# Optimization experiments

Hardware: AMD Instinct MI355X
Metric: run time of the kernel (lower is better)

The kernel has to match this reference:

```python
import jax, jax.numpy as jnp
import numpy as np


def _ln(x, g, b, eps=1e-5):
    m = x.mean(-1, keepdims=True)
    v = x.var(-1, keepdims=True)
    return (x - m) / jnp.sqrt(v + eps) * g + b


def _causal_linear_attn(q, k, v, eps=1e-3):
    # q, k, v: (b, h, n, d). Matches lucidrains causal_linear_attn with bucket_size=1:
    # q -> softmax over feature dim, k -> exp, inclusive cumsum of k and k(outer)v over n.
    dh = q.shape[-1]
    q = jax.nn.softmax(q, axis=-1) * (dh ** -0.5)
    k = jnp.exp(k)
    k_cum = jnp.cumsum(k, axis=2)                                  # (b,h,n,d)
    ctx = jnp.cumsum(k[..., :, None] * v[..., None, :], axis=2)    # (b,h,n,d,d) running sum of k_i v_i^T
    d_inv = 1.0 / jnp.clip(jnp.einsum('bhnd,bhnd->bhn', k_cum, q), eps, None)
    return jnp.einsum('bhnd,bhnde->bhne', q, ctx) * d_inv[..., None]


def reference(x, ln1_g, ln1_b, Wq, Wk, Wv, Wo, bo, ln2_g, ln2_b, W1, b1, W2, b2, n_heads):
    depth = Wq.shape[0]
    B, N, D = x.shape
    H = int(n_heads)
    dh = D // H
    for i in range(depth):
        # --- pre-norm linear self-attention block ---
        xn = _ln(x, ln1_g[i], ln1_b[i])
        q = (xn @ Wq[i]).reshape(B, N, H, dh).transpose(0, 2, 1, 3)
        k = (xn @ Wk[i]).reshape(B, N, H, dh).transpose(0, 2, 1, 3)
        v = (xn @ Wv[i]).reshape(B, N, H, dh).transpose(0, 2, 1, 3)
        a = _causal_linear_attn(q, k, v)
        a = a.transpose(0, 2, 1, 3).reshape(B, N, D)
        x = x + a @ Wo[i] + bo[i]
        # --- pre-norm feed-forward block (mult=4, exact GELU) ---
        xn = _ln(x, ln2_g[i], ln2_b[i])
        x = x + jax.nn.gelu(xn @ W1[i] + b1[i], approximate=False) @ W2[i] + b2[i]
    return x


def setup_inputs() -> dict:
    key = jax.random.key(0)
    ks = jax.random.split(key, 8)
    B, N, D, H, depth = 2, 2048, 1024, 16, 2
    FF = 4 * D
    s = D ** -0.5
    x = jax.random.normal(ks[0], (B, N, D), dtype=jnp.float32)
    Wq = jax.random.normal(ks[1], (depth, D, D), dtype=jnp.float32) * s
    Wk = jax.random.normal(ks[2], (depth, D, D), dtype=jnp.float32) * s
    Wv = jax.random.normal(ks[3], (depth, D, D), dtype=jnp.float32) * s
    Wo = jax.random.normal(ks[4], (depth, D, D), dtype=jnp.float32) * s
    W1 = jax.random.normal(ks[5], (depth, D, FF), dtype=jnp.float32) * s
    W2 = jax.random.normal(ks[6], (depth, FF, D), dtype=jnp.float32) * (FF ** -0.5)
    return dict(
        x=x,
        ln1_g=jnp.ones((depth, D), jnp.float32), ln1_b=jnp.zeros((depth, D), jnp.float32),
        Wq=Wq, Wk=Wk, Wv=Wv, Wo=Wo, bo=jnp.zeros((depth, D), jnp.float32),
        ln2_g=jnp.ones((depth, D), jnp.float32), ln2_b=jnp.zeros((depth, D), jnp.float32),
        W1=W1, b1=jnp.zeros((depth, FF), jnp.float32),
        W2=W2, b2=jnp.zeros((depth, D), jnp.float32),
        n_heads=H,
    )
```

## Files before the change

kernel.cpp:

```cpp
#include <hip/hip_runtime.h>
#include <cmath>

#define BB 2
#define SEQ 2048
#define DIM 1024
#define NH 16
#define DH 64
#define DEPTH 2
#define FFD 4096
#define CHK 64
#define NCHK (SEQ/CHK)
#define ROWS (BB*SEQ)
#define QKP (3*DIM)

typedef __bf16 bf16x8 __attribute__((ext_vector_type(8)));
typedef __bf16 bf16x4 __attribute__((ext_vector_type(4)));
typedef float  f32x4  __attribute__((ext_vector_type(4)));

#define AS1 __attribute__((address_space(1)))
#define AS3 __attribute__((address_space(3)))
#define FENCE() asm volatile("" ::: "memory")
#define WAIT_LGKM0_NOPIN() asm volatile("s_waitcnt lgkmcnt(0)" ::: "memory")

__device__ __forceinline__ float gelu_fast(float x) {
    float x3 = x * x * x;
    float y = 1.5957691216057308f * (x + 0.044715f * x3);
    return x * __builtin_amdgcn_rcpf(1.0f + __expf(-y));
}

__device__ __forceinline__ int swz128(int row, int col) {
    return row * 64 + (col ^ ((row & 7) << 3));
}

__device__ __forceinline__ void swz_tile(int bid, int NX, int NY, int& tx, int& ty) {
    int NB = NX * NY;
    int q = NB >> 3, r = NB & 7;
    int xcd = bid & 7, seq = bid >> 3;
    int start = (xcd < r) ? xcd * (q + 1) : r * (q + 1) + (xcd - r) * q;
    int wgid = start + seq;
    int g = 0, rem = wgid;
    int gw = (NX < 4) ? NX : 4;
    while (rem >= gw * NY) {
        rem -= gw * NY; g++;
        int left = NX - 4 * g;
        gw = left < 4 ? left : 4;
    }
    ty = rem / gw;
    tx = 4 * g + rem % gw;
}

__global__ __launch_bounds__(256) void ln_kernel(
    const float* __restrict__ x, const float* __restrict__ g,
    const float* __restrict__ b, __bf16* __restrict__ out)
{
    int row = blockIdx.x;
    const float4* xr = (const float4*)(x + (size_t)row * DIM);
    int t = threadIdx.x;
    float4 v = xr[t];
    float s  = v.x + v.y + v.z + v.w;
    float ss = v.x*v.x + v.y*v.y + v.z*v.z + v.w*v.w;
    #pragma unroll
    for (int off = 32; off > 0; off >>= 1) {
        s  += __shfl_down(s, off);
        ss += __shfl_down(ss, off);
    }
    __shared__ float wsum[4], wsq[4], stats[2];
    int wid = t >> 6, lane = t & 63;
    if (lane == 0) { wsum[wid] = s; wsq[wid] = ss; }
    __syncthreads();
    if (t == 0) {
        float S  = wsum[0] + wsum[1] + wsum[2] + wsum[3];
        float SS = wsq[0] + wsq[1] + wsq[2] + wsq[3];
        float mean = S * (1.0f / DIM);
        float var  = SS * (1.0f / DIM) - mean * mean;
        stats[0] = mean;
        stats[1] = rsqrtf(var + 1e-5f);
    }
    __syncthreads();
    float mean = stats[0], rstd = stats[1];
    float4 gv = ((const float4*)g)[t];
    float4 bv = ((const float4*)b)[t];
    bf16x4 o;
    o[0] = (__bf16)((v.x - mean) * rstd * gv.x + bv.x);
    o[1] = (__bf16)((v.y - mean) * rstd * gv.y + bv.y);
    o[2] = (__bf16)((v.z - mean) * rstd * gv.z + bv.z);
    o[3] = (__bf16)((v.w - mean) * rstd * gv.w + bv.w);
    *(bf16x4*)(out + (size_t)row * DIM + t * 4) = o;
}

__global__ __launch_bounds__(256) void transpose_all(
    const float* __restrict__ wq, const float* __restrict__ wk,
    const float* __restrict__ wv, const float* __restrict__ wo,
    const float* __restrict__ w1, const float* __restrict__ w2,
    __bf16* __restrict__ wqkt, __bf16* __restrict__ wot,
    __bf16* __restrict__ w1t, __bf16* __restrict__ w2t)
{
    int id = blockIdx.x;
    const float* W; __bf16* Wt; int K, N, txt, tyt;
    if (id < 4096) {
        int seg = id >> 10, r = id & 1023;
        K = DIM; N = DIM;
        txt = r & 31; tyt = r >> 5;
        W  = seg == 0 ? wq : seg == 1 ? wk : seg == 2 ? wv : wo;
        Wt = seg < 3 ? wqkt + (size_t)seg * DIM * DIM : wot;
    } else if (id < 8192) {
        int r = id - 4096;
        K = DIM; N = FFD;
        txt = r & 127; tyt = r >> 7;
        W = w1; Wt = w1t;
    } else {
        int r = id - 8192;
        K = FFD; N = DIM;
        txt = r & 31; tyt = r >> 5;
        W = w2; Wt = w2t;
    }
    __shared__ float tile[32][33];
    int bx = txt * 32, by = tyt * 32;
    int tx = threadIdx.x & 31, ty = threadIdx.x >> 5;
    #pragma unroll
    for (int i = 0; i < 32; i += 8)
        tile[ty + i][tx] = W[(size_t)(by + ty + i) * N + bx + tx];
    __syncthreads();
    #pragma unroll
    for (int i = 0; i < 32; i += 8)
        Wt[(size_t)(bx + ty + i) * K + by + tx] = (__bf16)tile[tx][ty + i];
}

__global__ __launch_bounds__(256) void transpose_v(
    const __bf16* __restrict__ qkv, __bf16* __restrict__ vT)
{
    __shared__ __bf16 tile[64 * 64];
    int bx = blockIdx.x;
    int by = blockIdx.y;
    int t = threadIdx.x;
    int r0 = t >> 3, sl = t & 7;
    #pragma unroll
    for (int i = 0; i < 2; i++) {
        int row = i * 32 + r0;
        bf16x8 d = *(const bf16x8*)(qkv + (size_t)(bx * 64 + row) * QKP + 2 * DIM + by * 64 + sl * 8);
        *(bf16x8*)&tile[row * 64 + ((sl ^ (row & 7)) << 3)] = d;
    }
    __syncthreads();
    #pragma unroll
    for (int i = 0; i < 2; i++) {
        int d = i * 32 + r0;
        int rbase = sl * 8;
        bf16x8 o;
        #pragma unroll
        for (int j = 0; j < 8; j++) {
            int rr = rbase + j;
            o[j] = tile[rr * 64 + (((((d >> 3)) ^ (rr & 7)) << 3) | (d & 7))];
        }
        *(bf16x8*)(vT + (size_t)(by * 64 + d) * ROWS + bx * 64 + rbase) = o;
    }
}

#define TBM 256
#define TBN 256
#define TBK 64
template<int MODE, int OUTBF>
__global__ __launch_bounds__(512) void gemm256(
    const __bf16* __restrict__ A, const __bf16* __restrict__ Bt,
    void* __restrict__ Cv, const float* __restrict__ bias,
    const float* __restrict__ res, int M, int N, int K, int Kp,
    int NXT, int NYT, int NS)
{
    __shared__ __bf16 lds[2][2][TBM * TBK];
    int nb = NXT * NYT;
    int sk = blockIdx.x / nb;
    int tx, ty;
    swz_tile(blockIdx.x % nb, NXT, NYT, tx, ty);
    if (NS > 1) {
        A  += (size_t)sk * K;
        Bt += (size_t)sk * K;
        Cv = (void*)((char*)Cv + (size_t)sk * M * N * (OUTBF ? 2 : 4));
    }
    const int bm = ty * TBM, bn = tx * TBN;
    const int t = threadIdx.x;
    const int l = t & 63, w = t >> 6;
    const int wm = w >> 2, wn = w & 3;
    const int lm = l & 15, lk = l >> 4;

    f32x4 acc[8][4] = {};
    const int nt = K / TBK;
    const int NIT = nt / 2;

    const int s7 = lm & 7;
    const int c0 = (lk ^ s7) << 3;
    const int c1 = ((4 ^ lk) ^ s7) << 3;
    const __bf16* pA[2][2] = {
        { &lds[0][0][(wm * 128 + lm) * 64 + c0], &lds[0][0][(wm * 128 + lm) * 64 + c1] },
        { &lds[1][0][(wm * 128 + lm) * 64 + c0], &lds[1][0][(wm * 128 + lm) * 64 + c1] } };
    const __bf16* pB[2][2] = {
        { &lds[0][1][(wn * 64 + lm) * 64 + c0], &lds[0][1][(wn * 64 + lm) * 64 + c1] },
        { &lds[1][1][(wn * 64 + lm) * 64 + c0], &lds[1][1][(wn * 64 + lm) * 64 + c1] } };

    const int srow0 = t >> 3;
    const int scol0 = ((t & 7) ^ (srow0 & 7)) * 8;
    const __bf16* gAb = A + (size_t)(bm + srow0) * Kp + scol0;
    const __bf16* gBb = Bt + (size_t)(bn + srow0) * Kp + scol0;
    const int ldsw = w * 512;

    auto STAGEH = [&](int bf, int mat, int hf, int kt) {
        const __bf16* srcb = mat ? gBb : gAb;
        #pragma unroll
        for (int i = 0; i < 2; i++) {
            __builtin_amdgcn_global_load_lds(
                (const AS1 void*)(srcb + (size_t)(hf * 128 + i * 64) * Kp + kt * 64),
                (AS3 void*)(&lds[bf][mat][(hf * 2 + i) * 4096 + ldsw]), 16, 0, 0);
        }
    };
    auto LDA = [&](int bf, int g, bf16x8* af) {
        #pragma unroll
        for (int j = 0; j < 4; j++) {
            af[j * 2 + 0] = *(const bf16x8*)(pA[bf][0] + (g * 4 + j) * 1024);
            af[j * 2 + 1] = *(const bf16x8*)(pA[bf][1] + (g * 4 + j) * 1024);
        }
    };
    auto LDB = [&](int bf, bf16x8* bfv) {
        #pragma unroll
        for (int n = 0; n < 4; n++) {
            bfv[n * 2 + 0] = *(const bf16x8*)(pB[bf][0] + n * 1024);
            bfv[n * 2 + 1] = *(const bf16x8*)(pB[bf][1] + n * 1024);
        }
    };
    auto MM = [&](int g, int ng, bf16x8* af, bf16x8* bfv) {
        __builtin_amdgcn_s_setprio(1);
        #pragma unroll
        for (int j = 0; j < 4; j++)
            #pragma unroll
            for (int nn = 0; nn < 2; nn++)
                #pragma unroll
                for (int kk = 0; kk < 2; kk++)
                    acc[g * 4 + j][ng * 2 + nn] = __builtin_amdgcn_mfma_f32_16x16x32_bf16(
                        af[j * 2 + kk], bfv[(ng * 2 + nn) * 2 + kk], acc[g * 4 + j][ng * 2 + nn], 0, 0, 0);
        __builtin_amdgcn_s_setprio(0);
    };

    STAGEH(0, 0, 0, 0); STAGEH(0, 0, 1, 0); STAGEH(0, 1, 0, 0); STAGEH(0, 1, 1, 0);
    STAGEH(1, 1, 0, 1); STAGEH(1, 1, 1, 1); STAGEH(1, 0, 0, 1);
    asm volatile("s_waitcnt vmcnt(6)" ::: "memory");
    __builtin_amdgcn_s_barrier();

    bf16x8 aF[8], bF[8];
    for (int it = 0; it < NIT; it++) {
        int T2 = 2 * it + 2, U2 = 2 * it + 3;
        LDA(0, 0, aF); LDB(0, bF);
        STAGEH(1, 0, 1, 2 * it + 1);
        FENCE(); __builtin_amdgcn_s_barrier();
        MM(0, 0, aF, bF);
        WAIT_LGKM0_NOPIN();
        FENCE(); __builtin_amdgcn_s_barrier();
        if (T2 < nt) STAGEH(0, 1, 0, T2);
        FENCE(); __builtin_amdgcn_s_barrier();
        MM(0, 1, aF, bF);
        FENCE(); __builtin_amdgcn_s_barrier();
        LDA(0, 1, aF);
        if (T2 < nt) STAGEH(0, 1, 1, T2);
        FENCE(); __builtin_amdgcn_s_barrier();
        MM(1, 1, aF, bF);
        FENCE(); __builtin_amdgcn_s_barrier();
        if (T2 < nt) {
            STAGEH(0, 0, 0, T2);
            asm volatile("s_waitcnt vmcnt(6)" ::: "memory");
        } else {
            asm volatile("s_waitcnt vmcnt(0)" ::: "memory");
        }
        __builtin_amdgcn_s_barrier();
        MM(1, 0, aF, bF);
        FENCE(); __builtin_amdgcn_s_barrier();
        LDA(1, 0, aF); LDB(1, bF);
        if (T2 < nt) STAGEH(0, 0, 1, T2);
        FENCE(); __builtin_amdgcn_s_barrier();
        MM(0, 0, aF, bF);
        WAIT_LGKM0_NOPIN();
        FENCE(); __builtin_amdgcn_s_barrier();
        if (U2 < nt) STAGEH(1, 1, 0, U2);
        FENCE(); __builtin_amdgcn_s_barrier();
        MM(0, 1, aF, bF);
        FENCE(); __builtin_amdgcn_s_barrier();
        LDA(1, 1, aF);
        if (U2 < nt) STAGEH(1, 1, 1, U2);
        FENCE(); __builtin_amdgcn_s_barrier();
        MM(1, 1, aF, bF);
        FENCE(); __builtin_amdgcn_s_barrier();
        if (U2 < nt) {
            STAGEH(1, 0, 0, U2);
            asm volatile("s_waitcnt vmcnt(6)" ::: "memory");
        } else {
            asm volatile("s_waitcnt vmcnt(0)" ::: "memory");
        }
        __builtin_amdgcn_s_barrier();
        MM(1, 0, aF, bF);
        FENCE(); __builtin_amdgcn_s_barrier();
    }

    #pragma unroll
    for (int m = 0; m < 8; m++) {
        #pragma unroll
        for (int n = 0; n < 4; n++) {
            int col = bn + wn * 64 + n * 16 + lm;
            #pragma unroll
            for (int r = 0; r < 4; r++) {
                int row = bm + wm * 128 + m * 16 + lk * 4 + r;
                float v = acc[m][n][r];
                if (MODE == 1) v += res[(size_t)row * N + col] + bias[col];
                if (MODE == 2) v = gelu_fast(v + bias[col]);
                if (OUTBF) ((__bf16*)Cv)[(size_t)row * N + col] = (__bf16)v;
                else       ((float*)Cv)[(size_t)row * N + col] = v;
            }
        }
    }
}

template<int DOLN>
__global__ __launch_bounds__(256) void reduce4ln(
    const __bf16* __restrict__ parts, const float* __restrict__ bias,
    float* __restrict__ x, const float* __restrict__ g,
    const float* __restrict__ b, __bf16* __restrict__ xn)
{
    const size_t PS = (size_t)ROWS * DIM;
    int row = blockIdx.x, t = threadIdx.x;
    size_t base = (size_t)row * DIM + t * 4;
    float4 xr = *(const float4*)(x + base);
    float4 bv = ((const float4*)bias)[t];
    float o0 = xr.x + bv.x, o1 = xr.y + bv.y, o2 = xr.z + bv.z, o3 = xr.w + bv.w;
    #pragma unroll
    for (int s = 0; s < 4; s++) {
        bf16x4 p = *(const bf16x4*)(parts + s * PS + base);
        o0 += (float)p[0]; o1 += (float)p[1]; o2 += (float)p[2]; o3 += (float)p[3];
    }
    float4 o = {o0, o1, o2, o3};
    *(float4*)(x + base) = o;
    if constexpr (DOLN) {
        float s  = o0 + o1 + o2 + o3;
        float ss = o0*o0 + o1*o1 + o2*o2 + o3*o3;
        #pragma unroll
        for (int off = 32; off > 0; off >>= 1) {
            s  += __shfl_down(s, off);
            ss += __shfl_down(ss, off);
        }
        __shared__ float wsum[4], wsq[4], stats[2];
        int wid = t >> 6, lane = t & 63;
        if (lane == 0) { wsum[wid] = s; wsq[wid] = ss; }
        __syncthreads();
        if (t == 0) {
            float S  = wsum[0] + wsum[1] + wsum[2] + wsum[3];
            float SS = wsq[0] + wsq[1] + wsq[2] + wsq[3];
            float mean = S * (1.0f / DIM);
            float var  = SS * (1.0f / DIM) - mean * mean;
            stats[0] = mean;
            stats[1] = rsqrtf(var + 1e-5f);
        }
        __syncthreads();
        float mean = stats[0], rstd = stats[1];
        float4 gv = ((const float4*)g)[t];
        float4 bvv = ((const float4*)b)[t];
        bf16x4 on;
        on[0] = (__bf16)((o0 - mean) * rstd * gv.x + bvv.x);
        on[1] = (__bf16)((o1 - mean) * rstd * gv.y + bvv.y);
        on[2] = (__bf16)((o2 - mean) * rstd * gv.z + bvv.z);
        on[3] = (__bf16)((o3 - mean) * rstd * gv.w + bvv.w);
        *(bf16x4*)(xn + base) = on;
    }
}

__global__ __launch_bounds__(256) void attn_local_m(
    const __bf16* __restrict__ qkv, const __bf16* __restrict__ vTg,
    float* __restrict__ KVT, float* __restrict__ Ksum)
{
    int blk = blockIdx.x;
    int c = blk % NCHK, bh = blk / NCHK;
    int b = bh / NH, h = bh % NH;
    __shared__ __bf16 ek_s[64 * 64];
    __shared__ __bf16 ekT_s[64 * 68];
    __shared__ float ksum_p[4][64];
    int t = threadIdx.x, w = t >> 6, l = t & 63;
    size_t rowbase = (size_t)(b * SEQ + c * CHK);

    {
        int m = t >> 2, dq = t & 3;
        const __bf16* kr = qkv + (rowbase + m) * QKP + DIM + h * DH + dq * 16;
        bf16x8 k0 = *(const bf16x8*)kr;
        bf16x8 k1 = *(const bf16x8*)(kr + 8);
        bf16x8 e0, e1;
        #pragma unroll
        for (int j = 0; j < 8; j++) {
            e0[j] = (__bf16)__expf((float)k0[j]);
            e1[j] = (__bf16)__expf((float)k1[j]);
        }
        *(bf16x8*)&ek_s[swz128(m, dq * 16)] = e0;
        *(bf16x8*)&ek_s[swz128(m, dq * 16 + 8)] = e1;
    }
    __syncthreads();
    {
        float kacc = 0.f;
        #pragma unroll
        for (int g = 0; g < 4; g++) {
            bf16x4 pk;
            #pragma unroll
            for (int j = 0; j < 4; j++) {
                __bf16 e = ek_s[swz128(w * 16 + g * 4 + j, l)];
                pk[j] = e;
                kacc += (float)e;
            }
            *(bf16x4*)&ekT_s[l * 68 + w * 16 + g * 4] = pk;
        }
        ksum_p[w][l] = kacc;
    }
    __syncthreads();
    f32x4 acc[4] = {};
    const __bf16* vbase = vTg + (size_t)(h * DH + w * 16 + (l & 15)) * ROWS
                        + (size_t)b * SEQ + c * CHK + (l >> 4) * 8;
    bf16x8 a0 = *(const bf16x8*)vbase;
    bf16x8 a1 = *(const bf16x8*)(vbase + 32);
    #pragma unroll
    for (int fn = 0; fn < 4; fn++) {
        int rbase = (fn * 16 + (l & 15)) * 68 + (l >> 4) * 8;
        bf16x4 b0a = *(const bf16x4*)&ekT_s[rbase];
        bf16x4 b0b = *(const bf16x4*)&ekT_s[rbase + 4];
        bf16x4 b1a = *(const bf16x4*)&ekT_s[rbase + 32];
        bf16x4 b1b = *(const bf16x4*)&ekT_s[rbase + 36];
        bf16x8 b0, b1;
        #pragma unroll
        for (int j = 0; j < 4; j++) {
            b0[j] = b0a[j]; b0[j + 4] = b0b[j];
            b1[j] = b1a[j]; b1[j + 4] = b1b[j];
        }
        acc[fn] = __builtin_amdgcn_mfma_f32_16x16x32_bf16(a0, b0, acc[fn], 0, 0, 0);
        acc[fn] = __builtin_amdgcn_mfma_f32_16x16x32_bf16(a1, b1, acc[fn], 0, 0, 0);
    }
    float* kvout = KVT + (size_t)(bh * NCHK + c) * (DH * DH);
    #pragma unroll
    for (int fn = 0; fn < 4; fn++)
        #pragma unroll
        for (int r = 0; r < 4; r++)
            kvout[(w * 16 + (l >> 4) * 4 + r) * DH + fn * 16 + (l & 15)] = acc[fn][r];
    if (t < 64) {
        float s = ksum_p[0][t] + ksum_p[1][t] + ksum_p[2][t] + ksum_p[3][t];
        Ksum[(size_t)(bh * NCHK + c) * DH + t] = s;
    }
}

__global__ __launch_bounds__(256) void attn_scan2(
    float* __restrict__ KV, float* __restrict__ Ksum)
{
    int bh = blockIdx.y;
    int bx = blockIdx.x;
    int t = threadIdx.x;
    if (bx < 16) {
        int elem = bx * 256 + t;
        float run = 0.f;
        for (int c = 0; c < NCHK; c++) {
            float* p = KV + ((size_t)(bh * NCHK + c)) * (DH * DH) + elem;
            float tmp = *p;
            *p = run;
            run += tmp;
        }
    } else if (t < DH) {
        float run = 0.f;
        for (int c = 0; c < NCHK; c++) {
            float* p = Ksum + ((size_t)(bh * NCHK + c)) * DH + t;
            float tmp = *p;
            *p = run;
            run += tmp;
        }
    }
}

__global__ __launch_bounds__(256) void attn_out_m(
    const __bf16* __restrict__ qkv, const __bf16* __restrict__ vTg,
    const float* __restrict__ KVT, const float* __restrict__ Ksum,
    __bf16* __restrict__ ag)
{
    int blk = blockIdx.x;
    int c = blk % NCHK, bh = blk / NCHK;
    int b = bh / NH, h = bh % NH;
    __shared__ __bf16 q_s[64 * 64];
    __shared__ __bf16 ek_s[64 * 64];
    __shared__ __bf16 s_s[64 * 64];
    __shared__ __bf16 kvT_s[64 * 64];
    __shared__ float denom_s[64];
    int t = threadIdx.x, w = t >> 6, l = t & 63;
    size_t rowbase = (size_t)(b * SEQ + c * CHK);

    {
        int i = t >> 2, dq = t & 3;
        const __bf16* qr = qkv + (rowbase + i) * QKP + h * DH + dq * 16;
        bf16x8 q0 = *(const bf16x8*)qr, q1 = *(const bf16x8*)(qr + 8);
        float qf[16];
        #pragma unroll
        for (int j = 0; j < 8; j++) { qf[j] = (float)q0[j]; qf[8 + j] = (float)q1[j]; }
        float mx = qf[0];
        #pragma unroll
        for (int j = 1; j < 16; j++) mx = fmaxf(mx, qf[j]);
        mx = fmaxf(mx, __shfl_xor(mx, 1));
        mx = fmaxf(mx, __shfl_xor(mx, 2));
        float ss = 0.f;
        #pragma unroll
        for (int j = 0; j < 16; j++) { qf[j] = __expf(qf[j] - mx); ss += qf[j]; }
        ss += __shfl_xor(ss, 1);
        ss += __shfl_xor(ss, 2);
        float sc = 0.125f / ss;
        bf16x8 o0, o1;
        #pragma unroll
        for (int j = 0; j < 8; j++) {
            o0[j] = (__bf16)(qf[j] * sc);
            o1[j] = (__bf16)(qf[8 + j] * sc);
        }
        *(bf16x8*)&q_s[swz128(i, dq * 16)] = o0;
        *(bf16x8*)&q_s[swz128(i, dq * 16 + 8)] = o1;
        const float* kp = Ksum + (size_t)(bh * NCHK + c) * DH + dq * 16;
        float dk = 0.f;
        #pragma unroll
        for (int j = 0; j < 16; j++) dk += (qf[j] * sc) * kp[j];
        dk += __shfl_xor(dk, 1);
        dk += __shfl_xor(dk, 2);
        if (dq == 0) denom_s[i] = dk;
    }
    {
        int m = t >> 2, dq = t & 3;
        const __bf16* kr = qkv + (rowbase + m) * QKP + DIM + h * DH + dq * 16;
        bf16x8 k0 = *(const bf16x8*)kr, k1 = *(const bf16x8*)(kr + 8);
        bf16x8 e0, e1;
        #pragma unroll
        for (int j = 0; j < 8; j++) {
            e0[j] = (__bf16)__expf((float)k0[j]);
            e1[j] = (__bf16)__expf((float)k1[j]);
        }
        *(bf16x8*)&ek_s[swz128(m, dq * 16)] = e0;
        *(bf16x8*)&ek_s[swz128(m, dq * 16 + 8)] = e1;
    }
    {
        int e = t >> 2, dq = t & 3;
        const float* kvr = KVT + (size_t)(bh * NCHK + c) * (DH * DH) + e * DH + dq * 16;
        bf16x8 o0, o1;
        #pragma unroll
        for (int j = 0; j < 8; j++) { o0[j] = (__bf16)kvr[j]; o1[j] = (__bf16)kvr[8 + j]; }
        *(bf16x8*)&kvT_s[swz128(e, dq * 16)] = o0;
        *(bf16x8*)&kvT_s[swz128(e, dq * 16 + 8)] = o1;
    }
    __syncthreads();

    bf16x8 bq0 = *(const bf16x8*)&q_s[swz128(w * 16 + (l & 15), (l >> 4) * 8)];
    bf16x8 bq1 = *(const bf16x8*)&q_s[swz128(w * 16 + (l & 15), 32 + (l >> 4) * 8)];
    int i_col = w * 16 + (l & 15);
    float dsum = 0.f;
    #pragma unroll
    for (int fm = 0; fm < 4; fm++) {
        bf16x8 ae0 = *(const bf16x8*)&ek_s[swz128(fm * 16 + (l & 15), (l >> 4) * 8)];
        bf16x8 ae1 = *(const bf16x8*)&ek_s[swz128(fm * 16 + (l & 15), 32 + (l >> 4) * 8)];
        f32x4 z = {};
        z = __builtin_amdgcn_mfma_f32_16x16x32_bf16(ae0, bq0, z, 0, 0, 0);
        z = __builtin_amdgcn_mfma_f32_16x16x32_bf16(ae1, bq1, z, 0, 0, 0);
        bf16x4 pk;
        #pragma unroll
        for (int r = 0; r < 4; r++) {
            int m = fm * 16 + (l >> 4) * 4 + r;
            float v = (m <= i_col) ? z[r] : 0.f;
            pk[r] = (__bf16)v;
            dsum += (float)pk[r];
        }
        *(bf16x4*)&s_s[swz128(i_col, fm * 16 + (l >> 4) * 4)] = pk;
    }
    dsum += __shfl_xor(dsum, 16);
    dsum += __shfl_xor(dsum, 32);
    if (l < 16) denom_s[w * 16 + l] += dsum;

    bf16x8 as0 = *(const bf16x8*)&s_s[swz128(w * 16 + (l & 15), (l >> 4) * 8)];
    bf16x8 as1 = *(const bf16x8*)&s_s[swz128(w * 16 + (l & 15), 32 + (l >> 4) * 8)];
    f32x4 oacc[4] = {};
    #pragma unroll
    for (int fn = 0; fn < 4; fn++) {
        const __bf16* vb = vTg + (size_t)(h * DH + fn * 16 + (l & 15)) * ROWS
                         + (size_t)b * SEQ + c * CHK + (l >> 4) * 8;
        bf16x8 bv0 = *(const bf16x8*)vb;
        bf16x8 bv1 = *(const bf16x8*)(vb + 32);
        bf16x8 bk0 = *(const bf16x8*)&kvT_s[swz128(fn * 16 + (l & 15), (l >> 4) * 8)];
        bf16x8 bk1 = *(const bf16x8*)&kvT_s[swz128(fn * 16 + (l & 15), 32 + (l >> 4) * 8)];
        f32x4 z = oacc[fn];
        z = __builtin_amdgcn_mfma_f32_16x16x32_bf16(as0, bv0, z, 0, 0, 0);
        z = __builtin_amdgcn_mfma_f32_16x16x32_bf16(as1, bv1, z, 0, 0, 0);
        z = __builtin_amdgcn_mfma_f32_16x16x32_bf16(bq0, bk0, z, 0, 0, 0);
        z = __builtin_amdgcn_mfma_f32_16x16x32_bf16(bq1, bk1, z, 0, 0, 0);
        oacc[fn] = z;
    }
    #pragma unroll
    for (int r = 0; r < 4; r++) {
        int i = w * 16 + (l >> 4) * 4 + r;
        float dinv = 1.0f / fmaxf(denom_s[i], 1e-3f);
        #pragma unroll
        for (int fn = 0; fn < 4; fn++)
            ag[(rowbase + i) * DIM + h * DH + fn * 16 + (l & 15)] = (__bf16)(oacc[fn][r] * dinv);
    }
}

extern "C" void kernel_launch(void* const* d_in, const int* in_sizes, int n_in,
                              void* d_out, int out_size, void* d_ws, size_t ws_size,
                              hipStream_t stream) {
    (void)in_sizes; (void)n_in; (void)out_size; (void)ws_size;
    const float* x_in  = (const float*)d_in[0];
    const float* ln1_g = (const float*)d_in[1];
    const float* ln1_b = (const float*)d_in[2];
    const float* Wq    = (const float*)d_in[3];
    const float* Wk    = (const float*)d_in[4];
    const float* Wv    = (const float*)d_in[5];
    const float* Wo    = (const float*)d_in[6];
    const float* bo    = (const float*)d_in[7];
    const float* ln2_g = (const float*)d_in[8];
    const float* ln2_b = (const float*)d_in[9];
    const float* W1    = (const float*)d_in[10];
    const float* b1    = (const float*)d_in[11];
    const float* W2    = (const float*)d_in[12];
    const float* b2    = (const float*)d_in[13];

    float* x = (float*)d_out;
    const size_t MB = 1024 * 1024;
    char* base = (char*)d_ws;

    __bf16* qkv    = (__bf16*)base;
    __bf16* partsO = (__bf16*)base;
    __bf16* h1     = (__bf16*)base;
    __bf16* vTg    = (__bf16*)(base + 24 * MB);
    __bf16* xn     = (__bf16*)(base + 32 * MB);
    __bf16* parts  = (__bf16*)(base + 32 * MB);
    __bf16* a      = (__bf16*)(base + 40 * MB);
    float*  KVT    = (float*)(base + 48 * MB);
    float*  Ks     = (float*)(base + 64 * MB);
    __bf16* wqkt   = (__bf16*)(base + 65 * MB);
    __bf16* wot    = (__bf16*)(base + 71 * MB);
    __bf16* w1t    = (__bf16*)(base + 73 * MB);
    __bf16* w2t    = (__bf16*)(base + 81 * MB);

    const size_t SZ = (size_t)ROWS * DIM;
    hipMemcpyAsync(x, x_in, SZ * sizeof(float), hipMemcpyDeviceToDevice, stream);

    dim3 gScan(17, BB * NH);
    dim3 gTv(ROWS / 64, DIM / 64);

    for (int l = 0; l < DEPTH; l++) {
        const float* wq = Wq + (size_t)l * DIM * DIM;
        const float* wk = Wk + (size_t)l * DIM * DIM;
        const float* wv = Wv + (size_t)l * DIM * DIM;
        const float* wo = Wo + (size_t)l * DIM * DIM;
        const float* w1 = W1 + (size_t)l * DIM * FFD;
        const float* w2 = W2 + (size_t)l * FFD * DIM;

        transpose_all<<<12288, 256, 0, stream>>>(wq, wk, wv, wo, w1, w2,
                                                 wqkt, wot, w1t, w2t);

        if (l == 0)
            ln_kernel<<<ROWS, 256, 0, stream>>>(x, ln1_g, ln1_b, xn);
        gemm256<0, 1><<<12 * 16, 512, 0, stream>>>(xn, wqkt, qkv, nullptr, nullptr,
                                                   ROWS, QKP, DIM, DIM, 12, 16, 1);
        transpose_v<<<gTv, 256, 0, stream>>>(qkv, vTg);
        attn_local_m<<<BB * NH * NCHK, 256, 0, stream>>>(qkv, vTg, KVT, Ks);
        attn_scan2<<<gScan, 256, 0, stream>>>(KVT, Ks);
        attn_out_m<<<BB * NH * NCHK, 256, 0, stream>>>(qkv, vTg, KVT, Ks, a);
        gemm256<0, 1><<<4 * 16 * 4, 512, 0, stream>>>(a, wot, partsO, nullptr, nullptr,
                                                      ROWS, DIM, DIM / 4, DIM, 4, 16, 4);
        reduce4ln<1><<<ROWS, 256, 0, stream>>>(partsO, bo + l * DIM, x,
                                               ln2_g + l * DIM, ln2_b + l * DIM, xn);

        gemm256<2, 1><<<16 * 16, 512, 0, stream>>>(xn, w1t, h1, b1 + l * FFD, nullptr,
                                                   ROWS, FFD, DIM, DIM, 16, 16, 1);
        gemm256<0, 1><<<4 * 16 * 4, 512, 0, stream>>>(h1, w2t, parts, nullptr, nullptr,
                                                      ROWS, DIM, FFD / 4, FFD, 4, 16, 4);
        if (l + 1 < DEPTH)
            reduce4ln<1><<<ROWS, 256, 0, stream>>>(parts, b2 + l * DIM, x,
                                                   ln1_g + (l + 1) * DIM,
                                                   ln1_b + (l + 1) * DIM, xn);
        else
            reduce4ln<0><<<ROWS, 256, 0, stream>>>(parts, b2 + l * DIM, x,
                                                   nullptr, nullptr, nullptr);
    }
}
```

Baseline: 399.2 us.

## Coarsen GEMM pipeline to two MFMA phases per K-tile with paired stage loads

The GEMM main loop previously ran four MFMA quarter-phases per K-tile, each bracketed by barriers, with one half-tile global-to-LDS stage load issued between them. It now runs two larger phases, each covering all four N sub-tiles for one A group, and issues the stage loads in pairs. The prologue and vmcnt thresholds are adjusted to match, and the explicit lgkmcnt wait is dropped. This halves the barrier count per iteration to cut synchronisation overhead, but it gives the scheduler fewer slots to interleave memory traffic with MFMA and changes how deep the prefetch runs.

```diff
diff --git a/kernel.cpp b/kernel.cpp
--- a/kernel.cpp
+++ b/kernel.cpp
@@ -20,7 +20,6 @@
 #define AS1 __attribute__((address_space(1)))
 #define AS3 __attribute__((address_space(3)))
 #define FENCE() asm volatile("" ::: "memory")
-#define WAIT_LGKM0_NOPIN() asm volatile("s_waitcnt lgkmcnt(0)" ::: "memory")
 
 __device__ __forceinline__ float gelu_fast(float x) {
     float x3 = x * x * x;
@@ -224,74 +223,56 @@
             bfv[n * 2 + 1] = *(const bf16x8*)(pB[bf][1] + n * 1024);
         }
     };
-    auto MM = [&](int g, int ng, bf16x8* af, bf16x8* bfv) {
+    auto MM2 = [&](int g, bf16x8* af, bf16x8* bfv) {
         __builtin_amdgcn_s_setprio(1);
         #pragma unroll
         for (int j = 0; j < 4; j++)
             #pragma unroll
-            for (int nn = 0; nn < 2; nn++)
+            for (int n = 0; n < 4; n++)
                 #pragma unroll
                 for (int kk = 0; kk < 2; kk++)
-                    acc[g * 4 + j][ng * 2 + nn] = __builtin_amdgcn_mfma_f32_16x16x32_bf16(
-                        af[j * 2 + kk], bfv[(ng * 2 + nn) * 2 + kk], acc[g * 4 + j][ng * 2 + nn], 0, 0, 0);
+                    acc[g * 4 + j][n] = __builtin_amdgcn_mfma_f32_16x16x32_bf16(
+                        af[j * 2 + kk], bfv[n * 2 + kk], acc[g * 4 + j][n], 0, 0, 0);
         __builtin_amdgcn_s_setprio(0);
     };
 
     STAGEH(0, 0, 0, 0); STAGEH(0, 0, 1, 0); STAGEH(0, 1, 0, 0); STAGEH(0, 1, 1, 0);
-    STAGEH(1, 1, 0, 1); STAGEH(1, 1, 1, 1); STAGEH(1, 0, 0, 1);
-    asm volatile("s_waitcnt vmcnt(6)" ::: "memory");
+    STAGEH(1, 1, 0, 1); STAGEH(1, 1, 1, 1);
+    asm volatile("s_waitcnt vmcnt(4)" ::: "memory");
     __builtin_amdgcn_s_barrier();
 
     bf16x8 aF[8], bF[8];
     for (int it = 0; it < NIT; it++) {
-        int T2 = 2 * it + 2, U2 = 2 * it + 3;
+        int u = 2 * it + 1, T2 = 2 * it + 2, U2 = 2 * it + 3;
         LDA(0, 0, aF); LDB(0, bF);
-        STAGEH(1, 0, 1, 2 * it + 1);
+        STAGEH(1, 0, 0, u); STAGEH(1, 0, 1, u);
         FENCE(); __builtin_amdgcn_s_barrier();
-        MM(0, 0, aF, bF);
-        WAIT_LGKM0_NOPIN();
-        FENCE(); __builtin_amdgcn_s_barrier();
-        if (T2 < nt) STAGEH(0, 1, 0, T2);
-        FENCE(); __builtin_amdgcn_s_barrier();
-        MM(0, 1, aF, bF);
+        MM2(0, aF, bF);
         FENCE(); __builtin_amdgcn_s_barrier();
         LDA(0, 1, aF);
-        if (T2 < nt) STAGEH(0, 1, 1, T2);
-        FENCE(); __builtin_amdgcn_s_barrier();
-        MM(1, 1, aF, bF);
-        FENCE(); __builtin_amdgcn_s_barrier();
         if (T2 < nt) {
-            STAGEH(0, 0, 0, T2);
-            asm volatile("s_waitcnt vmcnt(6)" ::: "memory");
+            STAGEH(0, 1, 0, T2); STAGEH(0, 1, 1, T2);
+            asm volatile("s_waitcnt vmcnt(4)" ::: "memory");
         } else {
             asm volatile("s_waitcnt vmcnt(0)" ::: "memory");
         }
         __builtin_amdgcn_s_barrier();
-        MM(1, 0, aF, bF);
+        MM2(1, aF, bF);
         FENCE(); __builtin_amdgcn_s_barrier();
         LDA(1, 0, aF); LDB(1, bF);
-        if (T2 < nt) STAGEH(0, 0, 1, T2);
+        if (T2 < nt) { STAGEH(0, 0, 0, T2); STAGEH(0, 0, 1, T2); }
         FENCE(); __builtin_amdgcn_s_barrier();
-        MM(0, 0, aF, bF);
-        WAIT_LGKM0_NOPIN();
-        FENCE(); __builtin_amdgcn_s_barrier();
-        if (U2 < nt) STAGEH(1, 1, 0, U2);
-        FENCE(); __builtin_amdgcn_s_barrier();
-        MM(0, 1, aF, bF);
+        MM2(0, aF, bF);
         FENCE(); __builtin_amdgcn_s_barrier();
         LDA(1, 1, aF);
-        if (U2 < nt) STAGEH(1, 1, 1, U2);
-        FENCE(); __builtin_amdgcn_s_barrier();
-        MM(1, 1, aF, bF);
-        FENCE(); __builtin_amdgcn_s_barrier();
         if (U2 < nt) {
-            STAGEH(1, 0, 0, U2);
-            asm volatile("s_waitcnt vmcnt(6)" ::: "memory");
+            STAGEH(1, 1, 0, U2); STAGEH(1, 1, 1, U2);
+            asm volatile("s_waitcnt vmcnt(4)" ::: "memory");
         } else {
             asm volatile("s_waitcnt vmcnt(0)" ::: "memory");
         }
         __builtin_amdgcn_s_barrier();
-        MM(1, 0, aF, bF);
+        MM2(1, aF, bF);
         FENCE(); __builtin_amdgcn_s_barrier();
     }
 
```

Result: no change. 395.5 us (-0.9%).
